# Optimization experiments

Measured on AMD Instinct MI355X. Metric: run time of the kernel, lower is better.

The kernel has to match this reference:

```python
import jax, jax.numpy as jnp
import numpy as np

ALPHA = 2.0  # snntorch ATan surrogate default

@jax.custom_vjp
def atan_spike(x):
    return (x > 0).astype(x.dtype)

def _atan_fwd(x):
    return (x > 0).astype(x.dtype), x

def _atan_bwd(x, g):
    return (g * (ALPHA / 2.0) / (1.0 + (jnp.pi / 2.0 * ALPHA * x) ** 2),)

atan_spike.defvjp(_atan_fwd, _atan_bwd)

def leaky_step(x, mem, beta, thr):
    # snntorch Leaky, reset_mechanism='subtract': reset from PREVIOUS mem (detached)
    b = jnp.clip(beta, 0.0, 1.0)
    reset = jax.lax.stop_gradient((mem - thr > 0).astype(mem.dtype))
    mem_new = b * mem + x - reset * thr
    spk = atan_spike(mem_new - thr)
    return spk, mem_new

B, D_IN, D_H, P = 4096, 2048, 2048, 1024

def setup_inputs() -> dict:
    key = jax.random.key(0)
    ks = jax.random.split(key, 32)
    def lin_params(k, fan_in, fan_out):
        bound = 1.0 / np.sqrt(fan_in)
        kw, kb = jax.random.split(k)
        W = jax.random.uniform(kw, (fan_out, fan_in), minval=-bound, maxval=bound, dtype=jnp.float32)
        b = jax.random.uniform(kb, (fan_out,), minval=-bound, maxval=bound, dtype=jnp.float32)
        return W, b
    inp = {}
    for n, i in zip(["spk_x_1", "spk_x_2", "spk_x_3", "spk_x_4", "hidden_prev"], range(5)):
        inp[n] = (jax.random.uniform(ks[i], (B, D_IN if i < 4 else D_H)) < 0.2).astype(jnp.float32)
    inp["syn_prev"] = jax.random.normal(ks[5], (B, D_H), dtype=jnp.float32)
    inp["mem_forget"] = jax.random.normal(ks[6], (B, P), dtype=jnp.float32)
    inp["mem_input"] = jax.random.normal(ks[7], (B, P), dtype=jnp.float32)
    inp["mem_gate"] = jax.random.normal(ks[8], (B, P), dtype=jnp.float32)
    inp["mem_output"] = jax.random.normal(ks[9], (B, P), dtype=jnp.float32)
    inp["mem_hidden"] = jax.random.normal(ks[10], (B, D_H), dtype=jnp.float32)
    names = [("Wif", D_IN), ("Whf", D_H), ("Wii", D_IN), ("Whi", D_H), ("Wig", D_IN), ("Whg", D_H), ("Wio", D_IN), ("Who", D_H)]
    for j, (n, fi) in enumerate(names):
        fo = P
        W, b = lin_params(ks[11 + j], fi, fo)
        inp[n + "_w"] = W
        inp[n + "_b"] = b
    for n in ["forget", "input", "gate", "output", "hidden"]:
        inp["beta_" + n] = jnp.float32(0.9)
        inp["thr_" + n] = jnp.float32(1.0)
    return inp

def reference(spk_x_1, spk_x_2, spk_x_3, spk_x_4, hidden_prev, syn_prev,
              mem_forget, mem_input, mem_gate, mem_output, mem_hidden,
              Wif_w, Wif_b, Whf_w, Whf_b, Wii_w, Wii_b, Whi_w, Whi_b,
              Wig_w, Wig_b, Whg_w, Whg_b, Wio_w, Wio_b, Who_w, Who_b,
              beta_forget, thr_forget, beta_input, thr_input, beta_gate, thr_gate,
              beta_output, thr_output, beta_hidden, thr_hidden):
    def lin(x, W, b):
        return x @ W.T + b
    enc_f = lin(spk_x_1, Wif_w, Wif_b) + lin(hidden_prev, Whf_w, Whf_b)
    spk_f, mem_f = leaky_step(enc_f, mem_forget, beta_forget, thr_forget)
    f = jax.nn.sigmoid(jnp.mean(spk_f, axis=1, keepdims=True))  # [B,1]
    enc_i = lin(spk_x_2, Wii_w, Wii_b) + lin(hidden_prev, Whi_w, Whi_b)
    spk_i, mem_i = leaky_step(enc_i, mem_input, beta_input, thr_input)
    i = jax.nn.sigmoid(jnp.mean(spk_i, axis=1, keepdims=True))
    enc_g = lin(spk_x_3, Wig_w, Wig_b) + lin(hidden_prev, Whg_w, Whg_b)
    spk_g, mem_g = leaky_step(enc_g, mem_gate, beta_gate, thr_gate)
    g = jnp.tanh(jnp.mean(spk_g, axis=1, keepdims=True))
    enc_o = lin(spk_x_4, Wio_w, Wio_b) + lin(hidden_prev, Who_w, Who_b)
    spk_o, mem_o = leaky_step(enc_o, mem_output, beta_output, thr_output)
    o = jax.nn.sigmoid(jnp.mean(spk_o, axis=1, keepdims=True))
    syn = f * syn_prev + i * g  # [B, D_H]
    mem_h_in = o * jnp.tanh(syn)
    hidden, mem_h = leaky_step(mem_h_in, mem_hidden, beta_hidden, thr_hidden)
    return (hidden, syn, mem_f, mem_i, mem_g, mem_o, mem_h)
```

## Files before the change

### kernel.cpp

```cpp
#include <hip/hip_runtime.h>

typedef int v4i __attribute__((ext_vector_type(4)));

#define OFF_SYN   8388608ull
#define OFF_MEM   16777216ull
#define OFF_MEMH  33554432ull
#define AQ01_BYTE  50331648ull
#define AQ234_BYTE 134217728ull
#define A_BYTES    8388608ull

struct PackArgs { const int4* src[5]; int4* dst[5]; };
struct WArgs    { const float* W1[4]; const float* W2[4]; signed char* Wq; };
struct GArgs {
  const signed char* ax[4];
  const signed char* ah;
  const signed char* Wq;
  const float* mem[4];
  const float* b1[4];
  const float* b2[4];
  const float* beta[4];
  const float* thr[4];
  float* out;
};
struct CArgs {
  const float* memo; const float* syn_prev; const float* mem_hidden;
  const float* thr[4]; const float* beta_h; const float* thr_h;
  float* hid; float* syn; float* memh;
};

__device__ __forceinline__ void gload16(const void* gsrc, void* lds) {
  __builtin_amdgcn_global_load_lds(
      (__attribute__((address_space(1))) void*)(gsrc),
      (__attribute__((address_space(3))) void*)(lds), 16, 0, 0);
}

__global__ __launch_bounds__(256) void k_pack(PackArgs a) {
  unsigned idx = blockIdx.x * 256u + threadIdx.x;
  unsigned arr = idx >> 19;
  unsigned off = idx & 524287u;
  const int4* s = a.src[arr] + (size_t)off * 4;
  int4 v0 = s[0], v1 = s[1], v2 = s[2], v3 = s[3];
  union { signed char c[16]; int4 v; } u;
  u.c[0]=(signed char)(v0.x!=0); u.c[1]=(signed char)(v0.y!=0);
  u.c[2]=(signed char)(v0.z!=0); u.c[3]=(signed char)(v0.w!=0);
  u.c[4]=(signed char)(v1.x!=0); u.c[5]=(signed char)(v1.y!=0);
  u.c[6]=(signed char)(v1.z!=0); u.c[7]=(signed char)(v1.w!=0);
  u.c[8]=(signed char)(v2.x!=0); u.c[9]=(signed char)(v2.y!=0);
  u.c[10]=(signed char)(v2.z!=0); u.c[11]=(signed char)(v2.w!=0);
  u.c[12]=(signed char)(v3.x!=0); u.c[13]=(signed char)(v3.y!=0);
  u.c[14]=(signed char)(v3.z!=0); u.c[15]=(signed char)(v3.w!=0);
  a.dst[arr][off] = u.v;
}

__global__ __launch_bounds__(256) void k_wdig(WArgs a) {
  unsigned idx = blockIdx.x * 256u + threadIdx.x;
  unsigned g  = idx >> 20;
  unsigned n  = (idx >> 10) & 1023u;
  unsigned kk = (idx & 1023u) << 2;
  const float* src = (kk < 2048u) ? (a.W1[g] + (size_t)n * 2048 + kk)
                                  : (a.W2[g] + (size_t)n * 2048 + (kk - 2048u));
  float4 w = *(const float4*)src;
  float wv[4] = {w.x, w.y, w.z, w.w};
  union { signed char c[4]; int i; } u0, u1, u2;
  #pragma unroll
  for (int e = 0; e < 4; ++e) {
    long long q = llrint((double)wv[e] * 268435456.0);
    long long r0 = ((q + 128) & 255) - 128; q = (q - r0) / 256;
    long long r1 = ((q + 128) & 255) - 128; q = (q - r1) / 256;
    u0.c[e] = (signed char)r0; u1.c[e] = (signed char)r1; u2.c[e] = (signed char)q;
  }
  size_t gb = (size_t)g * 3ull * 1024ull * 4096ull;
  size_t base = (size_t)n * 4096 + kk;
  *(int*)(a.Wq + gb + 0ull * 4194304ull + base) = u0.i;
  *(int*)(a.Wq + gb + 1ull * 4194304ull + base) = u1.i;
  *(int*)(a.Wq + gb + 2ull * 4194304ull + base) = u2.i;
}

__global__ __launch_bounds__(256, 2) void k_gemm(GArgs a) {
  __shared__ __align__(16) signed char As[4][128 * 64];
  __shared__ __align__(16) signed char Bs[4][3][64 * 64];
  const int tid = threadIdx.x;
  const int w = tid >> 6, l = tid & 63;
  const int wr = w >> 1, wc = w & 1;
  const int g = blockIdx.z, mt = blockIdx.y, nt = blockIdx.x;
  const int lr = l >> 2;
  const int lk = l & 3;

  v4i acc[3][4][2];
  v4i zero = {0, 0, 0, 0};
  #pragma unroll
  for (int d = 0; d < 3; ++d)
    #pragma unroll
    for (int mi = 0; mi < 4; ++mi)
      #pragma unroll
      for (int ni = 0; ni < 2; ++ni) acc[d][mi][ni] = zero;

  const signed char* Wg = a.Wq + (size_t)g * 3ull * 4194304ull
                               + (size_t)(nt * 64) * 4096ull;

  auto stage = [&](int buf, int t) {
    int K0 = t * 64;
    const signed char* Ab; int kl;
    if (K0 < 2048) { Ab = a.ax[g]; kl = K0; } else { Ab = a.ah; kl = K0 - 2048; }
    #pragma unroll
    for (int c = 0; c < 2; ++c) {
      int rl = ((w * 2 + c) << 4) + lr;
      int sw = (rl >> 1) & 3;
      gload16(Ab + (size_t)(mt * 128 + rl) * 2048 + kl + ((lk ^ sw) << 4),
              &As[buf][((w * 2 + c) << 4) * 64]);
    }
    #pragma unroll
    for (int d = 0; d < 3; ++d) {
      int rl = (w << 4) + lr;
      int sw = (rl >> 1) & 3;
      gload16(Wg + (size_t)d * 4194304ull + (size_t)rl * 4096ull + K0
                 + ((lk ^ sw) << 4),
              &Bs[buf][d][(w << 4) * 64]);
    }
  };

  auto step = [&](int t, bool pf, bool last) {
    if (last) asm volatile("s_waitcnt vmcnt(0)" ::: "memory");
    else      asm volatile("s_waitcnt vmcnt(5)" ::: "memory");
    __builtin_amdgcn_s_barrier();
    __builtin_amdgcn_sched_barrier(0);
    const int cur = t & 3;
    v4i av[4];
    #pragma unroll
    for (int mi = 0; mi < 4; ++mi) {
      int ar = wr * 64 + mi * 16 + (l & 15);
      int kg = (l >> 4) ^ ((ar >> 1) & 3);
      av[mi] = *(const v4i*)&As[cur][ar * 64 + kg * 16];
    }
    v4i bv[3][2];
    #pragma unroll
    for (int d = 0; d < 3; ++d)
      #pragma unroll
      for (int ni = 0; ni < 2; ++ni) {
        int br = wc * 32 + ni * 16 + (l & 15);
        int kg = (l >> 4) ^ ((br >> 1) & 3);
        bv[d][ni] = *(const v4i*)&Bs[cur][d][br * 64 + kg * 16];
      }
    if (pf) stage((t + 2) & 3, t + 2);
    __builtin_amdgcn_sched_barrier(0);
    __builtin_amdgcn_s_setprio(1);
    #pragma unroll
    for (int d = 0; d < 3; ++d)
      #pragma unroll
      for (int mi = 0; mi < 4; ++mi)
        #pragma unroll
        for (int ni = 0; ni < 2; ++ni)
          acc[d][mi][ni] = __builtin_amdgcn_mfma_i32_16x16x64_i8(
              av[mi], bv[d][ni], acc[d][mi][ni], 0, 0, 0);
    __builtin_amdgcn_s_setprio(0);
    __builtin_amdgcn_sched_barrier(0);
  };

  stage(0, 0);
  stage(1, 1);
  for (int t = 0; t < 62; ++t) step(t, true, false);
  step(62, false, false);
  step(63, false, true);

  const float* b1 = a.b1[g];
  const float* b2 = a.b2[g];
  const float* memg = a.mem[g];
  float* outg = a.out + (size_t)g * 4194304ull;
  double beta = fmin(fmax((double)(*a.beta[g]), 0.0), 1.0);
  double thr = (double)(*a.thr[g]);
  #pragma unroll
  for (int mi = 0; mi < 4; ++mi)
    #pragma unroll
    for (int ni = 0; ni < 2; ++ni) {
      int m0 = mt * 128 + wr * 64 + mi * 16 + ((l >> 4) << 2);
      int n  = nt * 64 + wc * 32 + ni * 16 + (l & 15);
      double bsum = (double)b1[n] + (double)b2[n];
      #pragma unroll
      for (int j = 0; j < 4; ++j) {
        double e = (double)acc[2][mi][ni][j] * 65536.0
                 + (double)acc[1][mi][ni][j] * 256.0
                 + (double)acc[0][mi][ni][j];
        double enc = e * (1.0 / 268435456.0) + bsum;
        size_t o = (size_t)(m0 + j) * 1024 + n;
        double mp = (double)memg[o];
        double reset = (mp - thr > 0.0) ? 1.0 : 0.0;
        double mn = beta * mp + enc - reset * thr;
        outg[o] = (float)mn;
      }
    }
}

__global__ __launch_bounds__(256) void k_fin(CArgs a) {
  const int b = blockIdx.x, tid = threadIdx.x;
  const int w = tid >> 6, l = tid & 63;
  __shared__ int scnt[4];
  __shared__ double sval[3];
  const float* mg = a.memo + (size_t)w * 4194304ull + (size_t)b * 1024;
  const float thrw = *a.thr[w];
  int cnt = 0;
  #pragma unroll
  for (int p = 0; p < 16; ++p) {
    float v = mg[l + p * 64];
    cnt += ((v - thrw) > 0.0f) ? 1 : 0;
  }
  #pragma unroll
  for (int off = 32; off; off >>= 1) cnt += __shfl_down(cnt, off, 64);
  if (l == 0) scnt[w] = cnt;
  __syncthreads();
  if (tid == 0) {
    double mf = scnt[0] * (1.0 / 1024.0);
    double mi = scnt[1] * (1.0 / 1024.0);
    double mgv = scnt[2] * (1.0 / 1024.0);
    double mo = scnt[3] * (1.0 / 1024.0);
    double f  = 1.0 / (1.0 + exp(-mf));
    double ii = 1.0 / (1.0 + exp(-mi));
    double gv = tanh(mgv);
    double oo = 1.0 / (1.0 + exp(-mo));
    sval[0] = f; sval[1] = ii * gv; sval[2] = oo;
  }
  __syncthreads();
  const double f = sval[0], ig = sval[1], oo = sval[2];
  const double bh = fmin(fmax((double)(*a.beta_h), 0.0), 1.0);
  const double th = (double)(*a.thr_h);
  const size_t rb = (size_t)b * 2048;
  for (int j = tid; j < 2048; j += 256) {
    double s = f * (double)a.syn_prev[rb + j] + ig;
    double mp = (double)a.mem_hidden[rb + j];
    double reset = (mp - th > 0.0) ? 1.0 : 0.0;
    double mh = bh * mp + oo * tanh(s) - reset * th;
    a.syn[rb + j] = (float)s;
    a.memh[rb + j] = (float)mh;
    a.hid[rb + j] = ((mh - th) > 0.0) ? 1.0f : 0.0f;
  }
}

extern "C" void kernel_launch(void* const* d_in, const int* in_sizes, int n_in,
                              void* d_out, int out_size, void* d_ws, size_t ws_size,
                              hipStream_t stream) {
  (void)in_sizes; (void)n_in; (void)out_size; (void)d_ws; (void)ws_size;
  float* out = (float*)d_out;
  signed char* base8 = (signed char*)d_out;

  PackArgs pa;
  for (int i = 0; i < 5; ++i) {
    pa.src[i] = (const int4*)d_in[i];
    pa.dst[i] = (int4*)(base8 + (i < 2 ? (AQ01_BYTE + (size_t)i * A_BYTES)
                                       : (AQ234_BYTE + (size_t)(i - 2) * A_BYTES)));
  }
  WArgs wa; wa.Wq = base8;
  for (int g = 0; g < 4; ++g) {
    wa.W1[g] = (const float*)d_in[11 + 4 * g];
    wa.W2[g] = (const float*)d_in[13 + 4 * g];
  }
  GArgs ga;
  for (int g = 0; g < 4; ++g) {
    ga.ax[g]   = (const signed char*)pa.dst[g];
    ga.mem[g]  = (const float*)d_in[6 + g];
    ga.b1[g]   = (const float*)d_in[12 + 4 * g];
    ga.b2[g]   = (const float*)d_in[14 + 4 * g];
    ga.beta[g] = (const float*)d_in[27 + 2 * g];
    ga.thr[g]  = (const float*)d_in[28 + 2 * g];
  }
  ga.ah = (const signed char*)pa.dst[4];
  ga.Wq = base8;
  ga.out = out + OFF_MEM;

  CArgs ca;
  ca.memo = out + OFF_MEM;
  ca.syn_prev = (const float*)d_in[5];
  ca.mem_hidden = (const float*)d_in[10];
  for (int g = 0; g < 4; ++g) ca.thr[g] = (const float*)d_in[28 + 2 * g];
  ca.beta_h = (const float*)d_in[35];
  ca.thr_h = (const float*)d_in[36];
  ca.hid = out;
  ca.syn = out + OFF_SYN;
  ca.memh = out + OFF_MEMH;

  k_pack<<<10240, 256, 0, stream>>>(pa);
  k_wdig<<<16384, 256, 0, stream>>>(wa);
  k_gemm<<<dim3(16, 32, 4), 256, 0, stream>>>(ga);
  k_fin<<<4096, 256, 0, stream>>>(ca);
}
```

Before: 382.8 us.

## Enlarge int8 GEMM tile to 128x128 with 8 waves and split-phase pipelining

The GEMM block grows from 256 to 512 threads with a 128x128 output tile, halving the grid in N so each A tile is reused across twice as many columns. Each K-step is split into two half-phases, each with its own LDS read, partial global prefetch and MFMA batch, separated by extra barriers. The aim is to cut global traffic per MFMA and interleave loads with compute more finely. LDS use doubles for B (roughly 128KB per block), which may limit occupancy to one block per CU despite the launch bound of 2. The extra barriers add sync cost.

```diff
diff --git a/kernel.cpp b/kernel.cpp
--- a/kernel.cpp
+++ b/kernel.cpp
@@ -76,12 +76,12 @@
   *(int*)(a.Wq + gb + 2ull * 4194304ull + base) = u2.i;
 }
 
-__global__ __launch_bounds__(256, 2) void k_gemm(GArgs a) {
+__global__ __launch_bounds__(512, 2) void k_gemm(GArgs a) {
   __shared__ __align__(16) signed char As[4][128 * 64];
-  __shared__ __align__(16) signed char Bs[4][3][64 * 64];
+  __shared__ __align__(16) signed char Bs[4][3][128 * 64];
   const int tid = threadIdx.x;
   const int w = tid >> 6, l = tid & 63;
-  const int wr = w >> 1, wc = w & 1;
+  const int wr = w >> 2, wc = w & 3;
   const int g = blockIdx.z, mt = blockIdx.y, nt = blockIdx.x;
   const int lr = l >> 2;
   const int lk = l & 3;
@@ -96,70 +96,92 @@
       for (int ni = 0; ni < 2; ++ni) acc[d][mi][ni] = zero;
 
   const signed char* Wg = a.Wq + (size_t)g * 3ull * 4194304ull
-                               + (size_t)(nt * 64) * 4096ull;
-
-  auto stage = [&](int buf, int t) {
+                               + (size_t)(nt * 128) * 4096ull;
+
+  auto stageP1 = [&](int buf, int t) {
     int K0 = t * 64;
     const signed char* Ab; int kl;
     if (K0 < 2048) { Ab = a.ax[g]; kl = K0; } else { Ab = a.ah; kl = K0 - 2048; }
-    #pragma unroll
-    for (int c = 0; c < 2; ++c) {
-      int rl = ((w * 2 + c) << 4) + lr;
-      int sw = (rl >> 1) & 3;
-      gload16(Ab + (size_t)(mt * 128 + rl) * 2048 + kl + ((lk ^ sw) << 4),
-              &As[buf][((w * 2 + c) << 4) * 64]);
-    }
-    #pragma unroll
-    for (int d = 0; d < 3; ++d) {
-      int rl = (w << 4) + lr;
-      int sw = (rl >> 1) & 3;
+    int rl = (w << 4) + lr;
+    int sw = (rl >> 1) & 3;
+    gload16(Ab + (size_t)(mt * 128 + rl) * 2048 + kl + ((lk ^ sw) << 4),
+            &As[buf][(w << 4) * 64]);
+    gload16(Wg + (size_t)rl * 4096ull + K0 + ((lk ^ sw) << 4),
+            &Bs[buf][0][(w << 4) * 64]);
+  };
+  auto stageP2 = [&](int buf, int t) {
+    int K0 = t * 64;
+    int rl = (w << 4) + lr;
+    int sw = (rl >> 1) & 3;
+    #pragma unroll
+    for (int d = 1; d < 3; ++d)
       gload16(Wg + (size_t)d * 4194304ull + (size_t)rl * 4096ull + K0
                  + ((lk ^ sw) << 4),
               &Bs[buf][d][(w << 4) * 64]);
-    }
   };
 
-  auto step = [&](int t, bool pf, bool last) {
-    if (last) asm volatile("s_waitcnt vmcnt(0)" ::: "memory");
-    else      asm volatile("s_waitcnt vmcnt(5)" ::: "memory");
-    __builtin_amdgcn_s_barrier();
-    __builtin_amdgcn_sched_barrier(0);
+  auto step = [&](int t, bool pf, bool drain) {
     const int cur = t & 3;
     v4i av[4];
+    v4i bv[3][2];
     #pragma unroll
     for (int mi = 0; mi < 4; ++mi) {
       int ar = wr * 64 + mi * 16 + (l & 15);
       int kg = (l >> 4) ^ ((ar >> 1) & 3);
       av[mi] = *(const v4i*)&As[cur][ar * 64 + kg * 16];
     }
-    v4i bv[3][2];
-    #pragma unroll
-    for (int d = 0; d < 3; ++d)
-      #pragma unroll
-      for (int ni = 0; ni < 2; ++ni) {
-        int br = wc * 32 + ni * 16 + (l & 15);
-        int kg = (l >> 4) ^ ((br >> 1) & 3);
-        bv[d][ni] = *(const v4i*)&Bs[cur][d][br * 64 + kg * 16];
-      }
-    if (pf) stage((t + 2) & 3, t + 2);
+    #pragma unroll
+    for (int d = 0; d < 3; ++d) {
+      int br = wc * 32 + (l & 15);
+      int kg = (l >> 4) ^ ((br >> 1) & 3);
+      bv[d][0] = *(const v4i*)&Bs[cur][d][br * 64 + kg * 16];
+    }
+    if (pf) stageP1((t + 2) & 3, t + 2);
+    __builtin_amdgcn_sched_barrier(0);
+    __builtin_amdgcn_s_barrier();
+    asm volatile("s_waitcnt lgkmcnt(0)" ::: "memory");
     __builtin_amdgcn_sched_barrier(0);
     __builtin_amdgcn_s_setprio(1);
     #pragma unroll
     for (int d = 0; d < 3; ++d)
       #pragma unroll
       for (int mi = 0; mi < 4; ++mi)
-        #pragma unroll
-        for (int ni = 0; ni < 2; ++ni)
-          acc[d][mi][ni] = __builtin_amdgcn_mfma_i32_16x16x64_i8(
-              av[mi], bv[d][ni], acc[d][mi][ni], 0, 0, 0);
+        acc[d][mi][0] = __builtin_amdgcn_mfma_i32_16x16x64_i8(
+            av[mi], bv[d][0], acc[d][mi][0], 0, 0, 0);
     __builtin_amdgcn_s_setprio(0);
     __builtin_amdgcn_sched_barrier(0);
+    __builtin_amdgcn_s_barrier();
+    #pragma unroll
+    for (int d = 0; d < 3; ++d) {
+      int br = wc * 32 + 16 + (l & 15);
+      int kg = (l >> 4) ^ ((br >> 1) & 3);
+      bv[d][1] = *(const v4i*)&Bs[cur][d][br * 64 + kg * 16];
+    }
+    if (pf) stageP2((t + 2) & 3, t + 2);
+    __builtin_amdgcn_sched_barrier(0);
+    __builtin_amdgcn_s_barrier();
+    asm volatile("s_waitcnt lgkmcnt(0)" ::: "memory");
+    __builtin_amdgcn_sched_barrier(0);
+    __builtin_amdgcn_s_setprio(1);
+    #pragma unroll
+    for (int d = 0; d < 3; ++d)
+      #pragma unroll
+      for (int mi = 0; mi < 4; ++mi)
+        acc[d][mi][1] = __builtin_amdgcn_mfma_i32_16x16x64_i8(
+            av[mi], bv[d][1], acc[d][mi][1], 0, 0, 0);
+    __builtin_amdgcn_s_setprio(0);
+    __builtin_amdgcn_sched_barrier(0);
+    if (drain) asm volatile("s_waitcnt vmcnt(0)" ::: "memory");
+    else       asm volatile("s_waitcnt vmcnt(4)" ::: "memory");
+    __builtin_amdgcn_s_barrier();
   };
 
-  stage(0, 0);
-  stage(1, 1);
+  stageP1(0, 0); stageP2(0, 0);
+  stageP1(1, 1); stageP2(1, 1);
+  asm volatile("s_waitcnt vmcnt(4)" ::: "memory");
+  __builtin_amdgcn_s_barrier();
   for (int t = 0; t < 62; ++t) step(t, true, false);
-  step(62, false, false);
+  step(62, false, true);
   step(63, false, true);
 
   const float* b1 = a.b1[g];
@@ -173,7 +195,7 @@
     #pragma unroll
     for (int ni = 0; ni < 2; ++ni) {
       int m0 = mt * 128 + wr * 64 + mi * 16 + ((l >> 4) << 2);
-      int n  = nt * 64 + wc * 32 + ni * 16 + (l & 15);
+      int n  = nt * 128 + wc * 32 + ni * 16 + (l & 15);
       double bsum = (double)b1[n] + (double)b2[n];
       #pragma unroll
       for (int j = 0; j < 4; ++j) {
@@ -278,6 +300,6 @@
 
   k_pack<<<10240, 256, 0, stream>>>(pa);
   k_wdig<<<16384, 256, 0, stream>>>(wa);
-  k_gemm<<<dim3(16, 32, 4), 256, 0, stream>>>(ga);
+  k_gemm<<<dim3(8, 32, 4), 512, 0, stream>>>(ga);
   k_fin<<<4096, 256, 0, stream>>>(ca);
 }
```

Measured after the change: 384.9 us. Within noise of the previous version (+0.5%).
